# Optimization experiments

Hardware: AMD Instinct MI355X
Metric: run time of the kernel (lower is better)

Reference implementation:

```python
import jax, jax.numpy as jnp
import numpy as np

BN_EPS = 1e-5

def _square_distance(a, b):
    # a: (B,N,3), b: (B,M,3) -> (B,N,M) squared euclidean distance
    a2 = jnp.sum(a * a, axis=-1)[:, :, None]
    b2 = jnp.sum(b * b, axis=-1)[:, None, :]
    return a2 + b2 - 2.0 * jnp.einsum('bnd,bmd->bnm', a, b)

def _bn(x, gamma, beta, mean, var):
    # eval-mode batchnorm over channel (last) dim
    return (x - mean) * jax.lax.rsqrt(var + BN_EPS) * gamma + beta

def setup_inputs() -> dict:
    key = jax.random.key(0)
    ks = jax.random.split(key, 16)
    B, M, N, D, C = 4, 2048, 16384, 64, 64
    din, dout = C + D, 64
    return {
        'xyz_down': jax.random.normal(ks[0], (B, M, 3), jnp.float32),
        'xyz_up': jax.random.normal(ks[1], (B, N, 3), jnp.float32),
        'feat_down': jax.random.normal(ks[2], (B, M, D), jnp.float32),
        'feat_up': jax.random.normal(ks[3], (B, N, C), jnp.float32),
        'W1': jax.random.normal(ks[4], (din, din), jnp.float32) * 0.05,
        'b1': jax.random.normal(ks[5], (din,), jnp.float32) * 0.05,
        'bn1_gamma': jax.random.uniform(ks[6], (din,), jnp.float32, 0.5, 1.5),
        'bn1_beta': jax.random.normal(ks[7], (din,), jnp.float32) * 0.05,
        'bn1_mean': jax.random.normal(ks[8], (din,), jnp.float32) * 0.05,
        'bn1_var': jax.random.uniform(ks[9], (din,), jnp.float32, 0.5, 1.5),
        'W2': jax.random.normal(ks[10], (dout, din), jnp.float32) * 0.05,
        'b2': jax.random.normal(ks[11], (dout,), jnp.float32) * 0.05,
        'bn2_gamma': jax.random.uniform(ks[12], (dout,), jnp.float32, 0.5, 1.5),
        'bn2_beta': jax.random.normal(ks[13], (dout,), jnp.float32) * 0.05,
        'bn2_mean': jax.random.normal(ks[14], (dout,), jnp.float32) * 0.05,
        'bn2_var': jax.random.uniform(ks[15], (dout,), jnp.float32, 0.5, 1.5),
    }

def reference(xyz_down, xyz_up, feat_down, feat_up,
              W1, b1, bn1_gamma, bn1_beta, bn1_mean, bn1_var,
              W2, b2, bn2_gamma, bn2_beta, bn2_mean, bn2_var):
    dist = _square_distance(xyz_up, xyz_down)              # (B,N,M)
    dist_recip = 1.0 / (dist + 1e-8)
    weight = dist_recip / jnp.sum(dist_recip, axis=2, keepdims=True)
    # bmm-equivalent of the original broadcast-multiply-sum
    feat_interp = jnp.einsum('bnm,bmd->bnd', weight, feat_down)  # (B,N,D)
    x = jnp.concatenate([feat_up, feat_interp], axis=-1)   # (B,N,C+D)
    # Conv1d(k=1) == pointwise linear over channel dim
    x = jnp.einsum('bnc,oc->bno', x, W1) + b1
    x = jax.nn.relu(_bn(x, bn1_gamma, bn1_beta, bn1_mean, bn1_var))
    x = jnp.einsum('bnc,oc->bno', x, W2) + b2
    x = _bn(x, bn2_gamma, bn2_beta, bn2_mean, bn2_var)
    return x
```

## Files before the change

kernel.cpp:

```cpp
#include <hip/hip_runtime.h>

typedef unsigned short u16;
typedef unsigned int   u32;
typedef unsigned long long u64;

typedef __attribute__((ext_vector_type(8))) short bf16x8;
typedef __attribute__((ext_vector_type(4))) float f32x4;
typedef __attribute__((ext_vector_type(2))) float f32x2;

#define BB 4
#define MM 2048
#define NN 16384
#define DD 64

__device__ __forceinline__ u16 f2bf(float f) {
    union { float f; u32 u; } v; v.f = f;
    u32 r = v.u + 0x7fffu + ((v.u >> 16) & 1u);
    return (u16)(r >> 16);
}

__device__ __forceinline__ u32 pack_trunc(float hi, float lo) {
    union { float f; u32 u; } a, b; a.f = hi; b.f = lo;
    return __builtin_amdgcn_perm(a.u, b.u, 0x07060302);
}

__device__ __forceinline__ u32 pack_rne(float hi, float lo) {
    return (u32)f2bf(lo) | ((u32)f2bf(hi) << 16);
}

__device__ __forceinline__ bf16x8 pack8(float4 p, float4 q) {
    bf16x8 v;
    v[0] = (short)f2bf(p.x); v[1] = (short)f2bf(p.y);
    v[2] = (short)f2bf(p.z); v[3] = (short)f2bf(p.w);
    v[4] = (short)f2bf(q.x); v[5] = (short)f2bf(q.y);
    v[6] = (short)f2bf(q.z); v[7] = (short)f2bf(q.w);
    return v;
}

#define OFF_FDT   0ull
#define OFF_XYZP  1048576ull
#define OFF_W1S   1179648ull
#define OFF_W2S   1212416ull
#define OFF_BN    1228800ull
#define WS_NEED   1230336ull

__global__ __launch_bounds__(256)
void prep6_kernel(const float* __restrict__ xyz_down,
                  const float* __restrict__ feat_down,
                  const float* __restrict__ W1, const float* __restrict__ b1,
                  const float* __restrict__ g1, const float* __restrict__ be1,
                  const float* __restrict__ m1, const float* __restrict__ v1,
                  const float* __restrict__ W2, const float* __restrict__ b2,
                  const float* __restrict__ g2, const float* __restrict__ be2,
                  const float* __restrict__ m2, const float* __restrict__ v2,
                  u16* __restrict__ fdT, float4* __restrict__ xyzP,
                  u16* __restrict__ w1s, u16* __restrict__ w2s,
                  float* __restrict__ bnbuf)
{
    const int blk = blockIdx.x, t = threadIdx.x;
    if (blk < 256) {
        __shared__ u16 T[32 * 72];
        const int b = blk >> 6, m0 = (blk & 63) * 32;
        {
            const int row = t >> 3, seg = (t & 7) * 8;
            const float4* src = (const float4*)(feat_down + ((size_t)(b * MM + m0 + row)) * 64 + seg);
            float4 v0 = src[0], v1 = src[1];
            bf16x8 pk = pack8(v0, v1);
            *(bf16x8*)&T[row * 72 + seg] = pk;
        }
        __syncthreads();
        {
            const int d = t & 63, w = t >> 6;
            union { u16 h[8]; uint4 q; } o;
#pragma unroll
            for (int j = 0; j < 8; j++) o.h[j] = T[(w * 8 + j) * 72 + d];
            *(uint4*)&fdT[((size_t)(b * 64 + d)) * MM + m0 + w * 8] = o.q;
        }
    } else if (blk < 272) {
        int g = (blk - 256) * 256 + t;
        int b = g >> 10, p = g & 1023;
        const float* s = xyz_down + ((size_t)b * MM + 2 * p) * 3;
        float x0 = s[0], y0 = s[1], z0 = s[2];
        float x1 = s[3], y1 = s[4], z1 = s[5];
        float w0 = x0 * x0 + y0 * y0 + z0 * z0 + 1e-8f;
        float w1v = x1 * x1 + y1 * y1 + z1 * z1 + 1e-8f;
        xyzP[(size_t)g * 2 + 0] = make_float4(-2.f * x0, -2.f * x1, -2.f * y0, -2.f * y1);
        xyzP[(size_t)g * 2 + 1] = make_float4(-2.f * z0, -2.f * z1, w0, w1v);
    } else if (blk < 280) {
        int slot = (blk - 272) * 256 + t;
        int f = slot >> 6, l = slot & 63;
        int kg = f >> 3, ot = f & 7;
        int o = ot * 16 + (l & 15), c = kg * 32 + (l >> 4) * 8;
        const float4* src = (const float4*)(W1 + (size_t)o * 128 + c);
        bf16x8 v = pack8(src[0], src[1]);
        *(bf16x8*)&w1s[(size_t)slot * 8] = v;
    } else if (blk < 284) {
        int slot = (blk - 280) * 256 + t;
        int f = slot >> 6, l = slot & 63;
        int kg = f >> 2, ot = f & 3;
        int o = ot * 16 + (l & 15), c = kg * 32 + (l >> 4) * 8;
        const float4* src = (const float4*)(W2 + (size_t)o * 128 + c);
        bf16x8 v = pack8(src[0], src[1]);
        *(bf16x8*)&w2s[(size_t)slot * 8] = v;
    } else {
        if (t < 128) {
            float a = g1[t] * rsqrtf(v1[t] + 1e-5f);
            bnbuf[t] = a;
            bnbuf[128 + t] = (b1[t] - m1[t]) * a + be1[t];
        } else if (t < 192) {
            int o = t - 128;
            float a = g2[o] * rsqrtf(v2[o] + 1e-5f);
            bnbuf[256 + o] = a;
            bnbuf[320 + o] = (b2[o] - m2[o]) * a + be2[o];
        }
    }
}

__global__ __launch_bounds__(512, 4)
void fused10_kernel(const float* __restrict__ xyz_up,
                    const u16* __restrict__ fdT,
                    const float4* __restrict__ xyzP,
                    const float* __restrict__ feat_up,
                    const u16* __restrict__ w1s,
                    const u16* __restrict__ w2s,
                    const float* __restrict__ bnbuf,
                    float* __restrict__ out)
{
    __shared__ __align__(16) char smem[34816];
    __shared__ float bnl[384];
    u16*   const ftbuf = (u16*)smem;
    float* const xyzb  = (float*)(smem + 18432);
    u16*   const xh    = (u16*)smem;
    float* const of    = (float*)smem;

    const int tid  = threadIdx.x;
    const int b    = blockIdx.x >> 7;
    const int n0   = (blockIdx.x & 127) * 128;
    const int wave = tid >> 6;
    const int lane = tid & 63;
    const int q    = lane >> 4;
    const int nl   = lane & 15;
    const int rg   = wave & 3;
    const int h    = wave >> 2;

    if (tid < 384) bnl[tid] = bnbuf[tid];

    float ax[2], ay[2], az[2];
    f32x2 a22[2];
#pragma unroll
    for (int rt = 0; rt < 2; rt++) {
        const int row = n0 + rg * 32 + rt * 16 + nl;
        const float* xu = xyz_up + ((size_t)(b * NN + row)) * 3;
        ax[rt] = xu[0]; ay[rt] = xu[1]; az[rt] = xu[2];
        float a2 = ax[rt] * ax[rt] + ay[rt] * ay[rt] + az[rt] * az[rt];
        a22[rt] = (f32x2){a2, a2};
    }
    const f32x2 eps2 = (f32x2){1e-8f, 1e-8f};

    f32x4 acc[2][4];
#pragma unroll
    for (int rt = 0; rt < 2; rt++)
#pragma unroll
        for (int i = 0; i < 4; i++) acc[rt][i] = (f32x4){0.f, 0.f, 0.f, 0.f};
    f32x4 accd[2];
    accd[0] = (f32x4){0.f, 0.f, 0.f, 0.f};
    accd[1] = (f32x4){0.f, 0.f, 0.f, 0.f};

    bf16x8 ones;
#pragma unroll
    for (int i = 0; i < 8; i++) ones[i] = (short)0x3F80;

    const int sd = tid >> 3, sms = (tid & 7) * 8;
    const u16* fsrc = fdT + ((size_t)(b * 64 + sd)) * MM + sms;
    const float4* xsrc = xyzP + ((size_t)b * 1024 + (tid >> 1)) * 2 + (tid & 1);
    const int xoff = (tid >> 1) * 12 + (tid & 1) * 4;

    uint4  rf;
    float4 rx;

    {
        uint4 f0v = *(const uint4*)(fsrc);
        *(uint4*)&ftbuf[sd * 72 + sms] = f0v;
        if (tid < 64) {
            float4 x0 = xsrc[0];
            *(float4*)&xyzb[xoff] = x0;
        }
        rf = *(const uint4*)(fsrc + 64);
        if (tid < 64) rx = xsrc[64];
        __builtin_amdgcn_sched_barrier(0);
        asm volatile("s_waitcnt lgkmcnt(0)" ::: "memory");
        __builtin_amdgcn_s_barrier();
        __builtin_amdgcn_sched_barrier(0);
    }

    int cur = 0;
    for (int c = 0; c < 32; ++c) {
        const int nxt = cur ^ 1;

        if (c + 1 < 32) {
            *(uint4*)&ftbuf[nxt * 4608 + sd * 72 + sms] = rf;
            if (tid < 64) *(float4*)&xyzb[nxt * 384 + xoff] = rx;
        }
        if (c + 2 < 32) {
            rf = *(const uint4*)(fsrc + (size_t)(c + 2) * 64);
            if (tid < 64) rx = xsrc[(size_t)(c + 2) * 64];
        }

        u32 fr[2][4];
#pragma unroll
        for (int jp = 0; jp < 4; jp++) {
            const int pi = h * 16 + q * 4 + jp;
            const float* base = &xyzb[cur * 384 + pi * 12];
            float4 ld0 = *(const float4*)(base);
            float4 ld1 = *(const float4*)(base + 4);
            f32x2 px = (f32x2){ld0.x, ld0.y};
            f32x2 py = (f32x2){ld0.z, ld0.w};
            f32x2 pz = (f32x2){ld1.x, ld1.y};
            f32x2 pw = (f32x2){ld1.z, ld1.w};
#pragma unroll
            for (int rt = 0; rt < 2; rt++) {
                f32x2 d = __builtin_elementwise_fma(px, (f32x2){ax[rt], ax[rt]},
                          __builtin_elementwise_fma(py, (f32x2){ay[rt], ay[rt]},
                          __builtin_elementwise_fma(pz, (f32x2){az[rt], az[rt]},
                                                    pw + a22[rt])));
                d = __builtin_elementwise_max(d, eps2);
                float r0 = __builtin_amdgcn_rcpf(d.x);
                float r1 = __builtin_amdgcn_rcpf(d.y);
                fr[rt][jp] = pack_trunc(r1, r0);
            }
        }
        bf16x8 bb[4];
#pragma unroll
        for (int dt = 0; dt < 4; dt++)
            bb[dt] = *(bf16x8*)&ftbuf[cur * 4608 + (dt * 16 + nl) * 72 + h * 32 + q * 8];
#pragma unroll
        for (int rt = 0; rt < 2; rt++) {
            union { u32 u[4]; bf16x8 v; } af;
            af.u[0] = fr[rt][0]; af.u[1] = fr[rt][1];
            af.u[2] = fr[rt][2]; af.u[3] = fr[rt][3];
#pragma unroll
            for (int dt = 0; dt < 4; dt++)
                acc[rt][dt] = __builtin_amdgcn_mfma_f32_16x16x32_bf16(af.v, bb[dt], acc[rt][dt], 0, 0, 0);
            accd[rt] = __builtin_amdgcn_mfma_f32_16x16x32_bf16(af.v, ones, accd[rt], 0, 0, 0);
        }

        __builtin_amdgcn_sched_barrier(0);
        asm volatile("s_waitcnt lgkmcnt(0)" ::: "memory");
        __builtin_amdgcn_s_barrier();
        __builtin_amdgcn_sched_barrier(0);
        cur = nxt;
    }

    const int fur = tid >> 2, fsg = (tid & 3) * 16;
    const float4* fup = (const float4*)(feat_up + ((size_t)(b * NN + n0 + fur)) * 64 + fsg);
    float4 f0 = fup[0], f1 = fup[1], f2 = fup[2], f3 = fup[3];

    if (h) {
#pragma unroll
        for (int rt = 0; rt < 2; rt++)
#pragma unroll
        for (int reg = 0; reg < 4; reg++) {
            int row = rg * 32 + rt * 16 + q * 4 + reg;
#pragma unroll
            for (int dt = 0; dt < 4; dt++)
                of[row * 68 + dt * 16 + nl] = acc[rt][dt][reg];
            if (nl == 0) of[row * 68 + 64] = accd[rt][reg];
        }
    }
    __syncthreads();
    if (!h) {
#pragma unroll
        for (int rt = 0; rt < 2; rt++)
#pragma unroll
        for (int reg = 0; reg < 4; reg++) {
            int row = rg * 32 + rt * 16 + q * 4 + reg;
#pragma unroll
            for (int dt = 0; dt < 4; dt++)
                acc[rt][dt][reg] += of[row * 68 + dt * 16 + nl];
            accd[rt][reg] += of[row * 68 + 64];
        }
    }
    __syncthreads();
    if (!h) {
#pragma unroll
        for (int rt = 0; rt < 2; rt++)
#pragma unroll
        for (int reg = 0; reg < 4; reg++) {
            float inv = 1.0f / accd[rt][reg];
            int row = rg * 32 + rt * 16 + q * 4 + reg;
#pragma unroll
            for (int dt = 0; dt < 4; dt++)
                xh[row * 136 + 64 + dt * 16 + nl] = f2bf(acc[rt][dt][reg] * inv);
        }
    }
    {
        uint4 o0, o1;
        o0.x = pack_rne(f0.y, f0.x); o0.y = pack_rne(f0.w, f0.z);
        o0.z = pack_rne(f1.y, f1.x); o0.w = pack_rne(f1.w, f1.z);
        o1.x = pack_rne(f2.y, f2.x); o1.y = pack_rne(f2.w, f2.z);
        o1.z = pack_rne(f3.y, f3.x); o1.w = pack_rne(f3.w, f3.z);
        uint4* xd = (uint4*)&xh[fur * 136 + fsg];
        xd[0] = o0; xd[1] = o1;
    }
    __syncthreads();

    f32x4 acc1[8];
#pragma unroll
    for (int i = 0; i < 8; i++) acc1[i] = (f32x4){0.f, 0.f, 0.f, 0.f};
#pragma unroll
    for (int kg = 0; kg < 4; kg++) {
        bf16x8 afr = *(bf16x8*)&xh[(wave * 16 + nl) * 136 + kg * 32 + q * 8];
#pragma unroll
        for (int ot = 0; ot < 8; ot++) {
            bf16x8 bf = *(const bf16x8*)(w1s + ((size_t)(kg * 8 + ot) * 64 + lane) * 8);
            acc1[ot] = __builtin_amdgcn_mfma_f32_16x16x32_bf16(afr, bf, acc1[ot], 0, 0, 0);
        }
    }
#pragma unroll
    for (int ot = 0; ot < 8; ot++) {
        int o = ot * 16 + nl;
        float aa = bnl[o], bc = bnl[128 + o];
#pragma unroll
        for (int reg = 0; reg < 4; reg++) {
            float v = fmaxf(fmaf(acc1[ot][reg], aa, bc), 0.f);
            xh[(wave * 16 + q * 4 + reg) * 136 + o] = f2bf(v);
        }
    }

    f32x4 acc2[4];
#pragma unroll
    for (int i = 0; i < 4; i++) acc2[i] = (f32x4){0.f, 0.f, 0.f, 0.f};
#pragma unroll
    for (int kg = 0; kg < 4; kg++) {
        bf16x8 afr = *(bf16x8*)&xh[(wave * 16 + nl) * 136 + kg * 32 + q * 8];
#pragma unroll
        for (int ot = 0; ot < 4; ot++) {
            bf16x8 bf = *(const bf16x8*)(w2s + ((size_t)(kg * 4 + ot) * 64 + lane) * 8);
            acc2[ot] = __builtin_amdgcn_mfma_f32_16x16x32_bf16(afr, bf, acc2[ot], 0, 0, 0);
        }
    }
#pragma unroll
    for (int ot = 0; ot < 4; ot++) {
        int o = ot * 16 + nl;
        float aa = bnl[256 + o], bc = bnl[320 + o];
#pragma unroll
        for (int reg = 0; reg < 4; reg++)
            of[(wave * 16 + q * 4 + reg) * 68 + o] = fmaf(acc2[ot][reg], aa, bc);
    }

    {
        const float4* sf = (const float4*)&of[fur * 68 + fsg];
        float4* dst = (float4*)(out + ((size_t)(b * NN + n0 + fur)) * 64 + fsg);
#pragma unroll
        for (int i = 0; i < 4; i++) dst[i] = sf[i];
    }
}

#define TN 128
#define BM 64
#define RS 72
#define FS 72

__global__ __launch_bounds__(256, 3)
void interp_kernel(const float* __restrict__ xyz_down,
                   const float* __restrict__ xyz_up,
                   const float* __restrict__ feat_down,
                   u16* __restrict__ interp_out)
{
    __shared__ u16   rbuf[TN * RS];
    __shared__ u16   ftbuf[DD * FS];
    __shared__ float xyzb[BM * 3];
    __shared__ float denp[TN * 2];
    __shared__ float invden[TN];

    const int tid = threadIdx.x;
    const int b  = blockIdx.x >> 7;
    const int n0 = (blockIdx.x & 127) * TN;

    const int nl_r = tid >> 1;
    const int half = tid & 1;
    const float* xu = xyz_up + (size_t)(b * NN + n0 + nl_r) * 3;
    const float ax = xu[0], ay = xu[1], az = xu[2];

    denp[tid] = 0.f;

    const int wave = tid >> 6;
    const int lane = tid & 63;
    const int q    = lane >> 4;
    const int nl   = lane & 15;

    f32x4 acc[2][4];
#pragma unroll
    for (int i = 0; i < 2; i++)
#pragma unroll
        for (int j = 0; j < 4; j++) acc[i][j] = (f32x4){0.f, 0.f, 0.f, 0.f};

    const int sm = (tid & 31) * 2;
    const int sd = (tid >> 5) * 8;

    for (int mc = 0; mc < MM; mc += BM) {
        __syncthreads();
        if (tid < 192) xyzb[tid] = xyz_down[(size_t)(b * MM + mc) * 3 + tid];
        {
            const float4* f0 = (const float4*)(feat_down + (size_t)(b * MM + mc + sm) * DD + sd);
            const float4* f1 = (const float4*)(feat_down + (size_t)(b * MM + mc + sm + 1) * DD + sd);
            float4 a0 = f0[0], a1 = f0[1];
            float4 b0 = f1[0], b1 = f1[1];
            float r0[8] = {a0.x, a0.y, a0.z, a0.w, a1.x, a1.y, a1.z, a1.w};
            float r1[8] = {b0.x, b0.y, b0.z, b0.w, b1.x, b1.y, b1.z, b1.w};
#pragma unroll
            for (int j = 0; j < 8; j++) {
                u32 pk = (u32)f2bf(r0[j]) | ((u32)f2bf(r1[j]) << 16);
                *(u32*)&ftbuf[(sd + j) * FS + sm] = pk;
            }
        }
        __syncthreads();
        {
            float dlc = 0.f;
#pragma unroll
            for (int s = 0; s < 4; s++) {
                bf16x8 v;
#pragma unroll
                for (int j = 0; j < 8; j++) {
                    int m = half * 32 + s * 8 + j;
                    float dx = ax - xyzb[3 * m + 0];
                    float dy = ay - xyzb[3 * m + 1];
                    float dz = az - xyzb[3 * m + 2];
                    float d = fmaf(dx, dx, fmaf(dy, dy, dz * dz)) + 1e-8f;
                    float r = __builtin_amdgcn_rcpf(d);
                    dlc += r;
                    v[j] = (short)f2bf(r);
                }
                *(bf16x8*)&rbuf[nl_r * RS + half * 32 + s * 8] = v;
            }
            denp[nl_r * 2 + half] += dlc;
        }
        __syncthreads();
        {
            const int rowbase = wave * 32;
#pragma unroll
            for (int k0 = 0; k0 < BM; k0 += 32) {
                bf16x8 a0 = *(bf16x8*)&rbuf[(rowbase + nl) * RS + k0 + q * 8];
                bf16x8 a1 = *(bf16x8*)&rbuf[(rowbase + 16 + nl) * RS + k0 + q * 8];
#pragma unroll
                for (int dt = 0; dt < 4; dt++) {
                    bf16x8 bb = *(bf16x8*)&ftbuf[(dt * 16 + nl) * FS + k0 + q * 8];
                    acc[0][dt] = __builtin_amdgcn_mfma_f32_16x16x32_bf16(a0, bb, acc[0][dt], 0, 0, 0);
                    acc[1][dt] = __builtin_amdgcn_mfma_f32_16x16x32_bf16(a1, bb, acc[1][dt], 0, 0, 0);
                }
            }
        }
    }

    __syncthreads();
    if (tid < TN) invden[tid] = 1.0f / (denp[tid * 2] + denp[tid * 2 + 1]);
    __syncthreads();
    {
        const int rowbase = wave * 32;
#pragma unroll
        for (int nt = 0; nt < 2; nt++) {
#pragma unroll
            for (int reg = 0; reg < 4; reg++) {
                int nloc = rowbase + nt * 16 + q * 4 + reg;
                float inv = invden[nloc];
                size_t gbase = (size_t)(b * NN + n0 + nloc) * DD;
#pragma unroll
                for (int dt = 0; dt < 4; dt++)
                    interp_out[gbase + dt * 16 + nl] = f2bf(acc[nt][dt][reg] * inv);
            }
        }
    }
}

#define T2 64

__global__ __launch_bounds__(256, 1)
void mlp_kernel(const float* __restrict__ feat_up,
                const u16*   __restrict__ interp,
                const float* __restrict__ W1, const float* __restrict__ b1,
                const float* __restrict__ g1, const float* __restrict__ be1,
                const float* __restrict__ m1, const float* __restrict__ v1,
                const float* __restrict__ W2, const float* __restrict__ b2,
                const float* __restrict__ g2, const float* __restrict__ be2,
                const float* __restrict__ m2, const float* __restrict__ v2,
                float* __restrict__ out)
{
    __shared__ u16 xb[T2 * 136];
    __shared__ u16 hb[T2 * 136];
    __shared__ u16 w1b[128 * 136];
    __shared__ u16 w2b[64 * 136];
    __shared__ float A1[128], Bc1[128], A2[64], Bc2[64];

    const int tid = threadIdx.x;
    const int b  = blockIdx.x >> 8;
    const int n0 = (blockIdx.x & 255) * T2;
    const int wave = tid >> 6;
    const int lane = tid & 63;
    const int q    = lane >> 4;
    const int nl   = lane & 15;

    if (tid < 128) {
        float a = g1[tid] * rsqrtf(v1[tid] + 1e-5f);
        A1[tid]  = a;
        Bc1[tid] = (b1[tid] - m1[tid]) * a + be1[tid];
    } else if (tid < 192) {
        int o = tid - 128;
        float a = g2[o] * rsqrtf(v2[o] + 1e-5f);
        A2[o]  = a;
        Bc2[o] = (b2[o] - m2[o]) * a + be2[o];
    }
    {
        const float4* src = (const float4*)(W1 + (size_t)(tid >> 1) * 128 + (tid & 1) * 64);
        u16* dst = &w1b[(tid >> 1) * 136 + (tid & 1) * 64];
#pragma unroll
        for (int i = 0; i < 8; i++)
            *(bf16x8*)(dst + 8 * i) = pack8(src[2 * i], src[2 * i + 1]);
    }
    {
        const float4* src = (const float4*)(W2 + (size_t)(tid >> 2) * 128 + (tid & 3) * 32);
        u16* dst = &w2b[(tid >> 2) * 136 + (tid & 3) * 32];
#pragma unroll
        for (int i = 0; i < 4; i++)
            *(bf16x8*)(dst + 8 * i) = pack8(src[2 * i], src[2 * i + 1]);
    }
    if (tid < 128) {
        int n = tid >> 1, hf = tid & 1;
        const float4* src = (const float4*)(feat_up + (size_t)(b * NN + n0 + n) * 64 + hf * 32);
        u16* dst = &xb[n * 136 + hf * 32];
#pragma unroll
        for (int i = 0; i < 4; i++)
            *(bf16x8*)(dst + 8 * i) = pack8(src[2 * i], src[2 * i + 1]);
    } else {
        int t2 = tid - 128;
        int n = t2 >> 1, hf = t2 & 1;
        const uint4* src = (const uint4*)(interp + (size_t)(b * NN + n0 + n) * 64 + hf * 32);
        u16* dst = &xb[n * 136 + 64 + hf * 32];
#pragma unroll
        for (int i = 0; i < 4; i++)
            *(uint4*)(dst + 8 * i) = src[i];
    }
    __syncthreads();

    f32x4 acc1[8];
#pragma unroll
    for (int i = 0; i < 8; i++) acc1[i] = (f32x4){0.f, 0.f, 0.f, 0.f};
#pragma unroll
    for (int k0 = 0; k0 < 128; k0 += 32) {
        bf16x8 a = *(bf16x8*)&xb[(wave * 16 + nl) * 136 + k0 + q * 8];
#pragma unroll
        for (int ot = 0; ot < 8; ot++) {
            bf16x8 bb = *(bf16x8*)&w1b[(ot * 16 + nl) * 136 + k0 + q * 8];
            acc1[ot] = __builtin_amdgcn_mfma_f32_16x16x32_bf16(a, bb, acc1[ot], 0, 0, 0);
        }
    }
#pragma unroll
    for (int ot = 0; ot < 8; ot++) {
        int o = ot * 16 + nl;
        float aa = A1[o], bc = Bc1[o];
#pragma unroll
        for (int reg = 0; reg < 4; reg++) {
            float v = fmaxf(fmaf(acc1[ot][reg], aa, bc), 0.f);
            hb[(wave * 16 + q * 4 + reg) * 136 + o] = f2bf(v);
        }
    }
    __syncthreads();

    f32x4 acc2[4];
#pragma unroll
    for (int i = 0; i < 4; i++) acc2[i] = (f32x4){0.f, 0.f, 0.f, 0.f};
#pragma unroll
    for (int k0 = 0; k0 < 128; k0 += 32) {
        bf16x8 a = *(bf16x8*)&hb[(wave * 16 + nl) * 136 + k0 + q * 8];
#pragma unroll
        for (int ot = 0; ot < 4; ot++) {
            bf16x8 bb = *(bf16x8*)&w2b[(ot * 16 + nl) * 136 + k0 + q * 8];
            acc2[ot] = __builtin_amdgcn_mfma_f32_16x16x32_bf16(a, bb, acc2[ot], 0, 0, 0);
        }
    }
#pragma unroll
    for (int ot = 0; ot < 4; ot++) {
        int o = ot * 16 + nl;
        float aa = A2[o], bc = Bc2[o];
#pragma unroll
        for (int reg = 0; reg < 4; reg++)
            out[(size_t)(b * NN + n0 + wave * 16 + q * 4 + reg) * 64 + o] =
                fmaf(acc2[ot][reg], aa, bc);
    }
}

extern "C" void kernel_launch(void* const* d_in, const int* in_sizes, int n_in,
                              void* d_out, int out_size, void* d_ws, size_t ws_size,
                              hipStream_t stream) {
    const float* xyz_down  = (const float*)d_in[0];
    const float* xyz_up    = (const float*)d_in[1];
    const float* feat_down = (const float*)d_in[2];
    const float* feat_up   = (const float*)d_in[3];
    const float* W1  = (const float*)d_in[4];
    const float* b1  = (const float*)d_in[5];
    const float* g1  = (const float*)d_in[6];
    const float* be1 = (const float*)d_in[7];
    const float* m1  = (const float*)d_in[8];
    const float* v1  = (const float*)d_in[9];
    const float* W2  = (const float*)d_in[10];
    const float* b2  = (const float*)d_in[11];
    const float* g2  = (const float*)d_in[12];
    const float* be2 = (const float*)d_in[13];
    const float* m2  = (const float*)d_in[14];
    const float* v2  = (const float*)d_in[15];
    float* out = (float*)d_out;
    char* ws = (char*)d_ws;

    if (ws_size >= WS_NEED) {
        u16*    fdT   = (u16*)(ws + OFF_FDT);
        float4* xyzP  = (float4*)(ws + OFF_XYZP);
        u16*    w1s   = (u16*)(ws + OFF_W1S);
        u16*    w2s   = (u16*)(ws + OFF_W2S);
        float*  bnbuf = (float*)(ws + OFF_BN);

        prep6_kernel<<<dim3(285), dim3(256), 0, stream>>>(
            xyz_down, feat_down, W1, b1, g1, be1, m1, v1,
            W2, b2, g2, be2, m2, v2, fdT, xyzP, w1s, w2s, bnbuf);
        fused10_kernel<<<dim3(BB * (NN / 128)), dim3(512), 0, stream>>>(
            xyz_up, fdT, xyzP, feat_up, w1s, w2s, bnbuf, out);
    } else {
        u16* interp = (u16*)d_ws;
        interp_kernel<<<dim3(BB * (NN / TN)), dim3(256), 0, stream>>>(
            xyz_down, xyz_up, feat_down, interp);
        mlp_kernel<<<dim3(BB * (NN / T2)), dim3(256), 0, stream>>>(
            feat_up, interp, W1, b1, g1, be1, m1, v1,
            W2, b2, g2, be2, m2, v2, out);
    }
}
```

Measured before the change: 146.3 us.

## Give each wave 64 rows over full M chunk, dropping split-K reduction

```diff
diff --git a/kernel.cpp b/kernel.cpp
--- a/kernel.cpp
+++ b/kernel.cpp
@@ -116,8 +116,8 @@
     }
 }
 
-__global__ __launch_bounds__(512, 4)
-void fused10_kernel(const float* __restrict__ xyz_up,
+__global__ __launch_bounds__(256, 1)
+void fused11_kernel(const float* __restrict__ xyz_up,
                     const u16* __restrict__ fdT,
                     const float4* __restrict__ xyzP,
                     const float* __restrict__ feat_up,
@@ -126,7 +126,7 @@
                     const float* __restrict__ bnbuf,
                     float* __restrict__ out)
 {
-    __shared__ __align__(16) char smem[34816];
+    __shared__ __align__(16) char smem[69632];
     __shared__ float bnl[384];
     u16*   const ftbuf = (u16*)smem;
     float* const xyzb  = (float*)(smem + 18432);
@@ -134,22 +134,22 @@
     float* const of    = (float*)smem;
 
     const int tid  = threadIdx.x;
-    const int b    = blockIdx.x >> 7;
-    const int n0   = (blockIdx.x & 127) * 128;
-    const int wave = tid >> 6;
+    const int b    = blockIdx.x >> 6;
+    const int n0   = (blockIdx.x & 63) * 256;
+    const int w    = tid >> 6;
     const int lane = tid & 63;
     const int q    = lane >> 4;
     const int nl   = lane & 15;
-    const int rg   = wave & 3;
-    const int h    = wave >> 2;
-
-    if (tid < 384) bnl[tid] = bnbuf[tid];
-
-    float ax[2], ay[2], az[2];
-    f32x2 a22[2];
-#pragma unroll
-    for (int rt = 0; rt < 2; rt++) {
-        const int row = n0 + rg * 32 + rt * 16 + nl;
+    const int wb   = w * 64;
+
+    bnl[tid] = bnbuf[tid];
+    if (tid < 128) bnl[256 + tid] = bnbuf[256 + tid];
+
+    float ax[4], ay[4], az[4];
+    f32x2 a22[4];
+#pragma unroll
+    for (int rt = 0; rt < 4; rt++) {
+        const int row = n0 + wb + rt * 16 + nl;
         const float* xu = xyz_up + ((size_t)(b * NN + row)) * 3;
         ax[rt] = xu[0]; ay[rt] = xu[1]; az[rt] = xu[2];
         float a2 = ax[rt] * ax[rt] + ay[rt] * ay[rt] + az[rt] * az[rt];
@@ -157,35 +157,38 @@
     }
     const f32x2 eps2 = (f32x2){1e-8f, 1e-8f};
 
-    f32x4 acc[2][4];
-#pragma unroll
-    for (int rt = 0; rt < 2; rt++)
+    f32x4 acc[4][4];
+#pragma unroll
+    for (int rt = 0; rt < 4; rt++)
 #pragma unroll
         for (int i = 0; i < 4; i++) acc[rt][i] = (f32x4){0.f, 0.f, 0.f, 0.f};
-    f32x4 accd[2];
-    accd[0] = (f32x4){0.f, 0.f, 0.f, 0.f};
-    accd[1] = (f32x4){0.f, 0.f, 0.f, 0.f};
+    f32x4 accd[4];
+#pragma unroll
+    for (int rt = 0; rt < 4; rt++) accd[rt] = (f32x4){0.f, 0.f, 0.f, 0.f};
 
     bf16x8 ones;
 #pragma unroll
     for (int i = 0; i < 8; i++) ones[i] = (short)0x3F80;
 
-    const int sd = tid >> 3, sms = (tid & 7) * 8;
+    const int sd = tid >> 2, sms = (tid & 3) * 16;
     const u16* fsrc = fdT + ((size_t)(b * 64 + sd)) * MM + sms;
     const float4* xsrc = xyzP + ((size_t)b * 1024 + (tid >> 1)) * 2 + (tid & 1);
     const int xoff = (tid >> 1) * 12 + (tid & 1) * 4;
 
-    uint4  rf;
+    uint4  rf0, rf1;
     float4 rx;
 
     {
-        uint4 f0v = *(const uint4*)(fsrc);
-        *(uint4*)&ftbuf[sd * 72 + sms] = f0v;
+        uint4 a0 = *(const uint4*)(fsrc);
+        uint4 a1 = *(const uint4*)(fsrc + 8);
+        *(uint4*)&ftbuf[sd * 72 + sms]     = a0;
+        *(uint4*)&ftbuf[sd * 72 + sms + 8] = a1;
         if (tid < 64) {
             float4 x0 = xsrc[0];
             *(float4*)&xyzb[xoff] = x0;
         }
-        rf = *(const uint4*)(fsrc + 64);
+        rf0 = *(const uint4*)(fsrc + 64);
+        rf1 = *(const uint4*)(fsrc + 72);
         if (tid < 64) rx = xsrc[64];
         __builtin_amdgcn_sched_barrier(0);
         asm volatile("s_waitcnt lgkmcnt(0)" ::: "memory");
@@ -198,50 +201,52 @@
         const int nxt = cur ^ 1;
 
         if (c + 1 < 32) {
-            *(uint4*)&ftbuf[nxt * 4608 + sd * 72 + sms] = rf;
+            *(uint4*)&ftbuf[nxt * 4608 + sd * 72 + sms]     = rf0;
+            *(uint4*)&ftbuf[nxt * 4608 + sd * 72 + sms + 8] = rf1;
             if (tid < 64) *(float4*)&xyzb[nxt * 384 + xoff] = rx;
         }
         if (c + 2 < 32) {
-            rf = *(const uint4*)(fsrc + (size_t)(c + 2) * 64);
+            rf0 = *(const uint4*)(fsrc + (size_t)(c + 2) * 64);
+            rf1 = *(const uint4*)(fsrc + (size_t)(c + 2) * 64 + 8);
             if (tid < 64) rx = xsrc[(size_t)(c + 2) * 64];
         }
 
-        u32 fr[2][4];
-#pragma unroll
-        for (int jp = 0; jp < 4; jp++) {
-            const int pi = h * 16 + q * 4 + jp;
-            const float* base = &xyzb[cur * 384 + pi * 12];
-            float4 ld0 = *(const float4*)(base);
-            float4 ld1 = *(const float4*)(base + 4);
-            f32x2 px = (f32x2){ld0.x, ld0.y};
-            f32x2 py = (f32x2){ld0.z, ld0.w};
-            f32x2 pz = (f32x2){ld1.x, ld1.y};
-            f32x2 pw = (f32x2){ld1.z, ld1.w};
-#pragma unroll
-            for (int rt = 0; rt < 2; rt++) {
-                f32x2 d = __builtin_elementwise_fma(px, (f32x2){ax[rt], ax[rt]},
-                          __builtin_elementwise_fma(py, (f32x2){ay[rt], ay[rt]},
-                          __builtin_elementwise_fma(pz, (f32x2){az[rt], az[rt]},
-                                                    pw + a22[rt])));
-                d = __builtin_elementwise_max(d, eps2);
-                float r0 = __builtin_amdgcn_rcpf(d.x);
-                float r1 = __builtin_amdgcn_rcpf(d.y);
-                fr[rt][jp] = pack_trunc(r1, r0);
-            }
-        }
-        bf16x8 bb[4];
-#pragma unroll
-        for (int dt = 0; dt < 4; dt++)
-            bb[dt] = *(bf16x8*)&ftbuf[cur * 4608 + (dt * 16 + nl) * 72 + h * 32 + q * 8];
-#pragma unroll
-        for (int rt = 0; rt < 2; rt++) {
-            union { u32 u[4]; bf16x8 v; } af;
-            af.u[0] = fr[rt][0]; af.u[1] = fr[rt][1];
-            af.u[2] = fr[rt][2]; af.u[3] = fr[rt][3];
+#pragma unroll
+        for (int kk = 0; kk < 2; kk++) {
+            bf16x8 bb[4];
 #pragma unroll
             for (int dt = 0; dt < 4; dt++)
-                acc[rt][dt] = __builtin_amdgcn_mfma_f32_16x16x32_bf16(af.v, bb[dt], acc[rt][dt], 0, 0, 0);
-            accd[rt] = __builtin_amdgcn_mfma_f32_16x16x32_bf16(af.v, ones, accd[rt], 0, 0, 0);
+                bb[dt] = *(bf16x8*)&ftbuf[cur * 4608 + (dt * 16 + nl) * 72 + kk * 32 + q * 8];
+#pragma unroll
+            for (int rt = 0; rt < 4; rt++) {
+                u32 fr[4];
+#pragma unroll
+                for (int jp = 0; jp < 4; jp++) {
+                    const int pi = kk * 16 + q * 4 + jp;
+                    const float* base = &xyzb[cur * 384 + pi * 12];
+                    float4 ld0 = *(const float4*)(base);
+                    float4 ld1 = *(const float4*)(base + 4);
+                    f32x2 px = (f32x2){ld0.x, ld0.y};
+                    f32x2 py = (f32x2){ld0.z, ld0.w};
+                    f32x2 pz = (f32x2){ld1.x, ld1.y};
+                    f32x2 pw = (f32x2){ld1.z, ld1.w};
+                    f32x2 d = __builtin_elementwise_fma(px, (f32x2){ax[rt], ax[rt]},
+                              __builtin_elementwise_fma(py, (f32x2){ay[rt], ay[rt]},
+                              __builtin_elementwise_fma(pz, (f32x2){az[rt], az[rt]},
+                                                        pw + a22[rt])));
+                    d = __builtin_elementwise_max(d, eps2);
+                    float r0 = __builtin_amdgcn_rcpf(d.x);
+                    float r1 = __builtin_amdgcn_rcpf(d.y);
+                    fr[jp] = pack_trunc(r1, r0);
+                }
+                union { u32 u[4]; bf16x8 v; } af;
+                af.u[0] = fr[0]; af.u[1] = fr[1];
+                af.u[2] = fr[2]; af.u[3] = fr[3];
+#pragma unroll
+                for (int dt = 0; dt < 4; dt++)
+                    acc[rt][dt] = __builtin_amdgcn_mfma_f32_16x16x32_bf16(af.v, bb[dt], acc[rt][dt], 0, 0, 0);
+                accd[rt] = __builtin_amdgcn_mfma_f32_16x16x32_bf16(af.v, ones, accd[rt], 0, 0, 0);
+            }
         }
 
         __builtin_amdgcn_sched_barrier(0);
@@ -251,108 +256,96 @@
         cur = nxt;
     }
 
-    const int fur = tid >> 2, fsg = (tid & 3) * 16;
-    const float4* fup = (const float4*)(feat_up + ((size_t)(b * NN + n0 + fur)) * 64 + fsg);
-    float4 f0 = fup[0], f1 = fup[1], f2 = fup[2], f3 = fup[3];
-
-    if (h) {
-#pragma unroll
-        for (int rt = 0; rt < 2; rt++)
-#pragma unroll
-        for (int reg = 0; reg < 4; reg++) {
-            int row = rg * 32 + rt * 16 + q * 4 + reg;
-#pragma unroll
-            for (int dt = 0; dt < 4; dt++)
-                of[row * 68 + dt * 16 + nl] = acc[rt][dt][reg];
-            if (nl == 0) of[row * 68 + 64] = accd[rt][reg];
-        }
-    }
     __syncthreads();
-    if (!h) {
-#pragma unroll
-        for (int rt = 0; rt < 2; rt++)
-#pragma unroll
-        for (int reg = 0; reg < 4; reg++) {
-            int row = rg * 32 + rt * 16 + q * 4 + reg;
-#pragma unroll
-            for (int dt = 0; dt < 4; dt++)
-                acc[rt][dt][reg] += of[row * 68 + dt * 16 + nl];
-            accd[rt][reg] += of[row * 68 + 64];
+
+#pragma unroll
+    for (int rt = 0; rt < 4; rt++)
+#pragma unroll
+    for (int reg = 0; reg < 4; reg++) {
+        float inv = 1.0f / accd[rt][reg];
+        int row = wb + rt * 16 + q * 4 + reg;
+#pragma unroll
+        for (int dt = 0; dt < 4; dt++)
+            xh[row * 136 + 64 + dt * 16 + nl] = f2bf(acc[rt][dt][reg] * inv);
+    }
+
+    {
+        const int fr_ = tid >> 2, fsg = (tid & 3) * 16;
+#pragma unroll
+        for (int p = 0; p < 4; p++) {
+            const int r = p * 64 + fr_;
+            const float4* fup = (const float4*)(feat_up + ((size_t)(b * NN + n0 + r)) * 64 + fsg);
+            float4 f0 = fup[0], f1 = fup[1], f2 = fup[2], f3 = fup[3];
+            uint4 o0, o1;
+            o0.x = pack_rne(f0.y, f0.x); o0.y = pack_rne(f0.w, f0.z);
+            o0.z = pack_rne(f1.y, f1.x); o0.w = pack_rne(f1.w, f1.z);
+            o1.x = pack_rne(f2.y, f2.x); o1.y = pack_rne(f2.w, f2.z);
+            o1.z = pack_rne(f3.y, f3.x); o1.w = pack_rne(f3.w, f3.z);
+            uint4* xd = (uint4*)&xh[r * 136 + fsg];
+            xd[0] = o0; xd[1] = o1;
         }
     }
     __syncthreads();
-    if (!h) {
-#pragma unroll
-        for (int rt = 0; rt < 2; rt++)
-#pragma unroll
-        for (int reg = 0; reg < 4; reg++) {
-            float inv = 1.0f / accd[rt][reg];
-            int row = rg * 32 + rt * 16 + q * 4 + reg;
-#pragma unroll
-            for (int dt = 0; dt < 4; dt++)
-                xh[row * 136 + 64 + dt * 16 + nl] = f2bf(acc[rt][dt][reg] * inv);
-        }
-    }
+
+#pragma unroll
+    for (int st = 0; st < 4; st++) {
+        const int rowA = wb + st * 16;
+
+        f32x4 acc1[8];
+#pragma unroll
+        for (int i = 0; i < 8; i++) acc1[i] = (f32x4){0.f, 0.f, 0.f, 0.f};
+#pragma unroll
+        for (int kg = 0; kg < 4; kg++) {
+            bf16x8 afr = *(bf16x8*)&xh[(rowA + nl) * 136 + kg * 32 + q * 8];
+#pragma unroll
+            for (int ot = 0; ot < 8; ot++) {
+                bf16x8 bf = *(const bf16x8*)(w1s + ((size_t)(kg * 8 + ot) * 64 + lane) * 8);
+                acc1[ot] = __builtin_amdgcn_mfma_f32_16x16x32_bf16(afr, bf, acc1[ot], 0, 0, 0);
+            }
+        }
+#pragma unroll
+        for (int ot = 0; ot < 8; ot++) {
+            int o = ot * 16 + nl;
+            float aa = bnl[o], bc = bnl[128 + o];
+#pragma unroll
+            for (int reg = 0; reg < 4; reg++) {
+                float v = fmaxf(fmaf(acc1[ot][reg], aa, bc), 0.f);
+                xh[(rowA + q * 4 + reg) * 136 + o] = f2bf(v);
+            }
+        }
+
+        f32x4 acc2[4];
+#pragma unroll
+        for (int i = 0; i < 4; i++) acc2[i] = (f32x4){0.f, 0.f, 0.f, 0.f};
+#pragma unroll
+        for (int kg = 0; kg < 4; kg++) {
+            bf16x8 afr = *(bf16x8*)&xh[(rowA + nl) * 136 + kg * 32 + q * 8];
+#pragma unroll
+            for (int ot = 0; ot < 4; ot++) {
+                bf16x8 bf = *(const bf16x8*)(w2s + ((size_t)(kg * 4 + ot) * 64 + lane) * 8);
+                acc2[ot] = __builtin_amdgcn_mfma_f32_16x16x32_bf16(afr, bf, acc2[ot], 0, 0, 0);
+            }
+        }
+#pragma unroll
+        for (int ot = 0; ot < 4; ot++) {
+            int o = ot * 16 + nl;
+            float aa = bnl[256 + o], bc = bnl[320 + o];
+#pragma unroll
+            for (int reg = 0; reg < 4; reg++)
+                of[(rowA + q * 4 + reg) * 68 + o] = fmaf(acc2[ot][reg], aa, bc);
+        }
+    }
+
     {
-        uint4 o0, o1;
-        o0.x = pack_rne(f0.y, f0.x); o0.y = pack_rne(f0.w, f0.z);
-        o0.z = pack_rne(f1.y, f1.x); o0.w = pack_rne(f1.w, f1.z);
-        o1.x = pack_rne(f2.y, f2.x); o1.y = pack_rne(f2.w, f2.z);
-        o1.z = pack_rne(f3.y, f3.x); o1.w = pack_rne(f3.w, f3.z);
-        uint4* xd = (uint4*)&xh[fur * 136 + fsg];
-        xd[0] = o0; xd[1] = o1;
-    }
-    __syncthreads();
-
-    f32x4 acc1[8];
-#pragma unroll
-    for (int i = 0; i < 8; i++) acc1[i] = (f32x4){0.f, 0.f, 0.f, 0.f};
-#pragma unroll
-    for (int kg = 0; kg < 4; kg++) {
-        bf16x8 afr = *(bf16x8*)&xh[(wave * 16 + nl) * 136 + kg * 32 + q * 8];
-#pragma unroll
-        for (int ot = 0; ot < 8; ot++) {
-            bf16x8 bf = *(const bf16x8*)(w1s + ((size_t)(kg * 8 + ot) * 64 + lane) * 8);
-            acc1[ot] = __builtin_amdgcn_mfma_f32_16x16x32_bf16(afr, bf, acc1[ot], 0, 0, 0);
-        }
-    }
-#pragma unroll
-    for (int ot = 0; ot < 8; ot++) {
-        int o = ot * 16 + nl;
-        float aa = bnl[o], bc = bnl[128 + o];
-#pragma unroll
-        for (int reg = 0; reg < 4; reg++) {
-            float v = fmaxf(fmaf(acc1[ot][reg], aa, bc), 0.f);
-            xh[(wave * 16 + q * 4 + reg) * 136 + o] = f2bf(v);
-        }
-    }
-
-    f32x4 acc2[4];
-#pragma unroll
-    for (int i = 0; i < 4; i++) acc2[i] = (f32x4){0.f, 0.f, 0.f, 0.f};
-#pragma unroll
-    for (int kg = 0; kg < 4; kg++) {
-        bf16x8 afr = *(bf16x8*)&xh[(wave * 16 + nl) * 136 + kg * 32 + q * 8];
-#pragma unroll
-        for (int ot = 0; ot < 4; ot++) {
-            bf16x8 bf = *(const bf16x8*)(w2s + ((size_t)(kg * 4 + ot) * 64 + lane) * 8);
-            acc2[ot] = __builtin_amdgcn_mfma_f32_16x16x32_bf16(afr, bf, acc2[ot], 0, 0, 0);
-        }
-    }
-#pragma unroll
-    for (int ot = 0; ot < 4; ot++) {
-        int o = ot * 16 + nl;
-        float aa = bnl[256 + o], bc = bnl[320 + o];
-#pragma unroll
-        for (int reg = 0; reg < 4; reg++)
-            of[(wave * 16 + q * 4 + reg) * 68 + o] = fmaf(acc2[ot][reg], aa, bc);
-    }
-
-    {
-        const float4* sf = (const float4*)&of[fur * 68 + fsg];
-        float4* dst = (float4*)(out + ((size_t)(b * NN + n0 + fur)) * 64 + fsg);
-#pragma unroll
-        for (int i = 0; i < 4; i++) dst[i] = sf[i];
+        const int rr = lane >> 2, sg = (lane & 3) * 16;
+#pragma unroll
+        for (int p = 0; p < 4; p++) {
+            const int r = wb + p * 16 + rr;
+            const float4* sf = (const float4*)&of[r * 68 + sg];
+            float4* dst = (float4*)(out + ((size_t)(b * NN + n0 + r)) * 64 + sg);
+#pragma unroll
+            for (int i = 0; i < 4; i++) dst[i] = sf[i];
+        }
     }
 }
 
@@ -620,7 +613,7 @@
         prep6_kernel<<<dim3(285), dim3(256), 0, stream>>>(
             xyz_down, feat_down, W1, b1, g1, be1, m1, v1,
             W2, b2, g2, be2, m2, v2, fdT, xyzP, w1s, w2s, bnbuf);
-        fused10_kernel<<<dim3(BB * (NN / 128)), dim3(512), 0, stream>>>(
+        fused11_kernel<<<dim3(BB * (NN / 256)), dim3(256), 0, stream>>>(
             xyz_up, fdT, xyzP, feat_up, w1s, w2s, bnbuf, out);
     } else {
         u16* interp = (u16*)d_ws;
```

Result: slower. 162.0 us (+10.7%).
